# Performance work log

Measured on AMD Instinct MI355X. Metric: run time of the kernel, lower is better.

The kernel has to match this reference:

```python
import jax, jax.numpy as jnp
import numpy as np

B, S, D = 4, 1024, 2048
H, KVH, HD = 32, 8, 64
N_REP = H // KVH  # 4
ROPE_THETA = 1000000.0


def _rope_tables(seq_len, head_dim, theta):
    inv_freq = 1.0 / (theta ** (np.arange(0, head_dim, 2, dtype=np.float32) / head_dim))
    t = np.arange(seq_len, dtype=np.float32)
    freqs = np.outer(t, inv_freq)                      # (S, HD/2)
    emb = np.concatenate([freqs, freqs], axis=-1)      # (S, HD)
    return jnp.asarray(np.cos(emb)), jnp.asarray(np.sin(emb))


def setup_inputs() -> dict:
    key = jax.random.key(0)
    kx, kq, kk, kv, ko = jax.random.split(key, 5)
    cos, sin = _rope_tables(S, HD, ROPE_THETA)
    s = 0.02
    return {
        "x": jax.random.normal(kx, (B, S, D), jnp.float32),
        "cos": cos,
        "sin": sin,
        "Wq": jax.random.normal(kq, (D, H * HD), jnp.float32) * s,
        "Wk": jax.random.normal(kk, (D, KVH * HD), jnp.float32) * s,
        "Wv": jax.random.normal(kv, (D, KVH * HD), jnp.float32) * s,
        "Wo": jax.random.normal(ko, (H * HD, D), jnp.float32) * s,
    }


def _rotate_half(t):
    t1, t2 = jnp.split(t, 2, axis=-1)
    return jnp.concatenate([-t2, t1], axis=-1)


def reference(x, cos, sin, Wq, Wk, Wv, Wo):
    # projections
    q = (x @ Wq).reshape(B, S, H, HD)      # (b, s, h, d)
    k = (x @ Wk).reshape(B, S, KVH, HD)
    v = (x @ Wv).reshape(B, S, KVH, HD)

    # RoPE: cos/sin (s, d) broadcast over heads (unsqueeze_dim=1 -> (s,1,d))
    c = cos[:, None, :]
    sn = sin[:, None, :]
    q = q * c + _rotate_half(q) * sn
    k = k * c + _rotate_half(k) * sn

    # GQA attention without physically repeating KV:
    # q grouped as (b, kvh, n_rep, s, d); repeat_kv '(h r)' maps q head g*n_rep+r -> kv head g
    qg = q.transpose(0, 2, 1, 3).reshape(B, KVH, N_REP, S, HD)
    kt = k.transpose(0, 2, 1, 3)  # (b, kvh, s, d)
    vt = v.transpose(0, 2, 1, 3)

    scale = 1.0 / jnp.sqrt(jnp.asarray(HD, x.dtype))
    scores = jnp.einsum('bgrqd,bgkd->bgrqk', qg, kt) * scale  # (b, kvh, rep, s, s)
    probs = jax.nn.softmax(scores, axis=-1)
    out = jnp.einsum('bgrqk,bgkd->bgrqd', probs, vt)           # (b, kvh, rep, s, d)

    out = out.reshape(B, H, S, HD).transpose(0, 2, 1, 3).reshape(B, S, H * HD)
    return out @ Wo
```

## Files before the change

### kernel.cpp

```cpp
#include <hip/hip_runtime.h>

typedef unsigned short u16;
typedef __attribute__((ext_vector_type(8))) __bf16 bf16x8;
typedef __attribute__((ext_vector_type(4))) _Float16 f16x4;
typedef __attribute__((ext_vector_type(8))) _Float16 f16x8;
typedef __attribute__((ext_vector_type(4))) float f32x4;

#define BB 4
#define SS 1024
#define DD 2048
#define HH 32
#define KVHN 8
#define HDIM 64

__device__ __forceinline__ u16 f2b(float f) {
    union { float f; unsigned u; } v; v.f = f;
    unsigned r = v.u + 0x7FFFu + ((v.u >> 16) & 1u);
    return (u16)(r >> 16);
}
__device__ __forceinline__ float b2f(u16 h) {
    union { unsigned u; float f; } v; v.u = ((unsigned)h) << 16; return v.f;
}

__device__ __forceinline__ f32x4 mfma16(bf16x8 a, bf16x8 b, f32x4 c) {
    return __builtin_amdgcn_mfma_f32_16x16x32_bf16(a, b, c, 0, 0, 0);
}
__device__ __forceinline__ f32x4 mfma16h(f16x8 a, f16x8 b, f32x4 c) {
    return __builtin_amdgcn_mfma_f32_16x16x32_f16(a, b, c, 0, 0, 0);
}

__device__ __forceinline__ void async_cp16(const void* g, void* l) {
    __builtin_amdgcn_global_load_lds((__attribute__((address_space(1))) void*)g,
                                     (__attribute__((address_space(3))) void*)l,
                                     16, 0, 0);
}

__device__ __forceinline__ void block_sync() {
    asm volatile("" ::: "memory");
    __builtin_amdgcn_s_barrier();
    asm volatile("" ::: "memory");
}

__device__ __forceinline__ f16x8 pack8_f16(const float* p) {
    union { unsigned u[4]; f16x8 v; } pu;
    pu.u[0] = __builtin_bit_cast(unsigned, __builtin_amdgcn_cvt_pkrtz(p[0], p[1]));
    pu.u[1] = __builtin_bit_cast(unsigned, __builtin_amdgcn_cvt_pkrtz(p[2], p[3]));
    pu.u[2] = __builtin_bit_cast(unsigned, __builtin_amdgcn_cvt_pkrtz(p[4], p[5]));
    pu.u[3] = __builtin_bit_cast(unsigned, __builtin_amdgcn_cvt_pkrtz(p[6], p[7]));
    return pu.v;
}

__global__ __launch_bounds__(256) void prep_kernel(const float* __restrict__ x,
                                                   const float* __restrict__ Wq,
                                                   const float* __restrict__ Wk,
                                                   const float* __restrict__ Wv,
                                                   const float* __restrict__ Wo,
                                                   u16* __restrict__ xb,
                                                   u16* __restrict__ Wqkvt,
                                                   u16* __restrict__ Wot) {
    __shared__ float tile[32][33];
    int z = blockIdx.z;
    int tid = threadIdx.x;
    if (z == 4) {
        int lb = blockIdx.y * 64 + blockIdx.x;
        int i = (lb * 256 + tid) * 8;
        float4 v0 = *(const float4*)(x + i);
        float4 v1 = *(const float4*)(x + i + 4);
        uint4 r;
        r.x = (unsigned)f2b(v0.x) | ((unsigned)f2b(v0.y) << 16);
        r.y = (unsigned)f2b(v0.z) | ((unsigned)f2b(v0.w) << 16);
        r.z = (unsigned)f2b(v1.x) | ((unsigned)f2b(v1.y) << 16);
        r.w = (unsigned)f2b(v1.z) | ((unsigned)f2b(v1.w) << 16);
        *(uint4*)(xb + i) = r;
        return;
    }
    const float* W = (z == 0) ? Wq : (z == 1) ? Wk : (z == 2) ? Wv : Wo;
    int N = (z == 1 || z == 2) ? 512 : 2048;
    int n_off = (z == 1) ? 2048 : (z == 2) ? 2560 : 0;
    u16* Wt = (z == 3) ? Wot : Wqkvt;
    int n0 = blockIdx.x * 32;
    if (n0 >= N) return;
    int k0 = blockIdx.y * 32;
    int nj = tid & 31;
    int ki = tid >> 5;
#pragma unroll
    for (int it = 0; it < 4; it++) {
        int kk = it * 8 + ki;
        tile[kk][nj] = W[(size_t)(k0 + kk) * N + n0 + nj];
    }
    __syncthreads();
    int kp = tid & 15;
    int nn8 = tid >> 4;
#pragma unroll
    for (int pass = 0; pass < 2; pass++) {
        int nn = pass * 16 + nn8;
        unsigned v = (unsigned)f2b(tile[kp * 2][nn]) |
                     ((unsigned)f2b(tile[kp * 2 + 1][nn]) << 16);
        *(unsigned*)&Wt[(size_t)(n0 + nn + n_off) * 2048 + k0 + kp * 2] = v;
    }
}

__global__ __launch_bounds__(512, 2) void gemm_qkv(const u16* __restrict__ A,
                                                   const u16* __restrict__ Bt,
                                                   const float* __restrict__ cosT,
                                                   const float* __restrict__ sinT,
                                                   u16* __restrict__ Qh,
                                                   u16* __restrict__ Kh,
                                                   u16* __restrict__ Vbuf) {
    __shared__ __align__(16) u16 Ls[2][32768];
    const int tid = threadIdx.x;
    const int lane = tid & 63;
    const int w = tid >> 6;

    const int bid = blockIdx.x;
    const int xcd = bid & 7;
    const int loc = bid >> 3;
    const int mt = (xcd & 3) * 4 + (loc & 3);
    const int nt = (xcd >> 2) * 6 + (loc >> 2);
    const int m0 = mt * 256;
    const int n0 = nt * 256;

    const int wm_h = w >> 2;
    const int wn = (w & 3) * 64;
    const int lr = lane & 15;
    const int lg = lane >> 4;

    const int sr = lane >> 3;
    const int sl = (lane & 7) ^ (sr & 7);
    const u16* pA = A + (size_t)(m0 + w * 8 + sr) * 2048 + sl * 8;
    const u16* pB = Bt + (size_t)(n0 + w * 8 + sr) * 2048 + sl * 8;

#define STA(buf_, h_, kt_)                                                               \
    {                                                                                    \
        async_cp16(pA + (size_t)((h_) * 128) * 2048 + (kt_) * 64, &Ls[buf_][(h_) * 8192 + w * 512]);            \
        async_cp16(pA + (size_t)((h_) * 128 + 64) * 2048 + (kt_) * 64, &Ls[buf_][(h_) * 8192 + 4096 + w * 512]); \
    }
#define STB(buf_, h_, kt_)                                                               \
    {                                                                                    \
        async_cp16(pB + (size_t)((h_) * 128) * 2048 + (kt_) * 64, &Ls[buf_][16384 + (h_) * 8192 + w * 512]);            \
        async_cp16(pB + (size_t)((h_) * 128 + 64) * 2048 + (kt_) * 64, &Ls[buf_][16384 + (h_) * 8192 + 4096 + w * 512]); \
    }

    f32x4 acc[8][4];
    const f32x4 zero4 = {0.f, 0.f, 0.f, 0.f};
#pragma unroll
    for (int i = 0; i < 8; i++)
#pragma unroll
        for (int j = 0; j < 4; j++) acc[i][j] = zero4;

    bf16x8 af[8], b0[4], b1[4];

#define LDA(mh_, buf_)                                                                   \
    _Pragma("unroll") for (int mi = 0; mi < 4; mi++) _Pragma("unroll") for (int ks = 0; ks < 2; ks++) { \
        int rh = (mh_) * 64 + mi * 16 + lr;                                              \
        af[mi * 2 + ks] = *(const bf16x8*)(&Ls[buf_][wm_h * 8192 + rh * 64 + (((ks * 4 + lg) ^ (lr & 7)) * 8)]); \
    }
#define LDB(dst_, nh_, buf_)                                                             \
    _Pragma("unroll") for (int ni = 0; ni < 2; ni++) _Pragma("unroll") for (int ks = 0; ks < 2; ks++) { \
        int rowb = wn + (nh_) * 32 + ni * 16 + lr;                                       \
        dst_[ni * 2 + ks] = *(const bf16x8*)(&Ls[buf_][16384 + (rowb >> 7) * 8192 + (rowb & 127) * 64 + (((ks * 4 + lg) ^ (lr & 7)) * 8)]); \
    }
#define QMM(mh_, nh_, bb_)                                                               \
    __builtin_amdgcn_s_setprio(1);                                                       \
    _Pragma("unroll") for (int mi = 0; mi < 4; mi++) _Pragma("unroll") for (int ni = 0; ni < 2; ni++) { \
        acc[(mh_) * 4 + mi][(nh_) * 2 + ni] = mfma16(af[mi * 2 + 0], bb_[ni * 2 + 0], acc[(mh_) * 4 + mi][(nh_) * 2 + ni]); \
        acc[(mh_) * 4 + mi][(nh_) * 2 + ni] = mfma16(af[mi * 2 + 1], bb_[ni * 2 + 1], acc[(mh_) * 4 + mi][(nh_) * 2 + ni]); \
    }                                                                                    \
    __builtin_amdgcn_s_setprio(0);
#define WAITLDS                                                                          \
    asm volatile("s_waitcnt lgkmcnt(0)" ::: "memory");                                   \
    __builtin_amdgcn_sched_barrier(0);

    STA(0, 0, 0); STA(0, 1, 0); STB(0, 0, 0); STB(0, 1, 0);
    STB(1, 0, 1); STB(1, 1, 1);
    asm volatile("s_waitcnt vmcnt(0)" ::: "memory");
    block_sync();

#pragma unroll 1
    for (int I = 0; I < 16; ++I) {
        const int tb = 2 * I + 1;
        const int ta2 = (2 * I + 2) & 31;
        const int tb2 = (2 * I + 3) & 31;

        LDA(0, 0); LDB(b0, 0, 0);
        STA(1, 0, tb);
        block_sync(); WAITLDS;
        QMM(0, 0, b0);
        block_sync();

        LDB(b1, 1, 0);
        STA(1, 1, tb);
        block_sync(); WAITLDS;
        QMM(0, 1, b1);
        block_sync();

        LDA(1, 0);
        STB(0, 0, ta2);
        block_sync(); WAITLDS;
        QMM(1, 1, b1);
        block_sync();

        STB(0, 1, ta2);
        block_sync(); WAITLDS;
        QMM(1, 0, b0);
        asm volatile("s_waitcnt vmcnt(4)" ::: "memory");
        block_sync();

        LDA(0, 1); LDB(b0, 0, 1);
        STA(0, 0, ta2);
        block_sync(); WAITLDS;
        QMM(0, 0, b0);
        block_sync();

        LDB(b1, 1, 1);
        STA(0, 1, ta2);
        block_sync(); WAITLDS;
        QMM(0, 1, b1);
        block_sync();

        LDA(1, 1);
        STB(1, 0, tb2);
        block_sync(); WAITLDS;
        QMM(1, 1, b1);
        block_sync();

        STB(1, 1, tb2);
        block_sync(); WAITLDS;
        QMM(1, 0, b0);
        asm volatile("s_waitcnt vmcnt(4)" ::: "memory");
        block_sync();
    }
    asm volatile("s_waitcnt vmcnt(0)" ::: "memory");

    const int lq = lg * 4;
    const int wm = wm_h * 128;
    const int hb = (n0 + wn) >> 6;

    if (hb < 32) {
        const float QSC = 0.125f * 1.44269504088896f;
#pragma unroll
        for (int mi = 0; mi < 8; mi++)
#pragma unroll
            for (int i = 0; i < 4; i++) {
                int r = m0 + wm + mi * 16 + lq + i;
                int s = r & (SS - 1);
                int b = r >> 10;
                const float* cb = cosT + s * HDIM;
                const float* sb = sinT + s * HDIM;
                u16* drow = Qh + ((size_t)(b * HH + hb) * SS + s) * HDIM;
#pragma unroll
                for (int p = 0; p < 2; p++) {
                    int dlo = p * 16 + lr;
                    float c = cb[dlo], sn = sb[dlo];
                    float alo = acc[mi][p][i], ahi = acc[mi][p + 2][i];
                    drow[dlo]      = f2b((alo * c - ahi * sn) * QSC);
                    drow[dlo + 32] = f2b((ahi * c + alo * sn) * QSC);
                }
            }
    } else if (hb < 40) {
        int g = hb - 32;
#pragma unroll
        for (int mi = 0; mi < 8; mi++)
#pragma unroll
            for (int i = 0; i < 4; i++) {
                int r = m0 + wm + mi * 16 + lq + i;
                int s = r & (SS - 1);
                int b = r >> 10;
                int rr = s & 7;
                int kpos = (s & ~31) + ((rr >= 4) ? 16 : 0) + ((s >> 3) & 3) * 4 + (rr & 3);
                const float* cb = cosT + s * HDIM;
                const float* sb = sinT + s * HDIM;
                u16* drow = Kh + ((size_t)(b * KVHN + g) * SS + kpos) * HDIM;
#pragma unroll
                for (int p = 0; p < 2; p++) {
                    int dlo = p * 16 + lr;
                    float c = cb[dlo], sn = sb[dlo];
                    float alo = acc[mi][p][i], ahi = acc[mi][p + 2][i];
                    drow[dlo]      = f2b(alo * c - ahi * sn);
                    drow[dlo + 32] = f2b(ahi * c + alo * sn);
                }
            }
    } else {
        int cv0 = (n0 + wn) - 2560;
#pragma unroll
        for (int mi = 0; mi < 8; mi++)
#pragma unroll
            for (int ni = 0; ni < 4; ni++)
#pragma unroll
                for (int i = 0; i < 4; i++) {
                    int r = m0 + wm + mi * 16 + lq + i;
                    union { _Float16 h; u16 u; } cvu;
                    cvu.h = (_Float16)acc[mi][ni][i];
                    Vbuf[(size_t)r * 512 + cv0 + ni * 16 + lr] = cvu.u;
                }
    }
#undef STA
#undef STB
#undef LDA
#undef LDB
#undef QMM
#undef WAITLDS
}

__global__ __launch_bounds__(512, 2) void gemm_out(const u16* __restrict__ A,
                                                   const u16* __restrict__ Bt,
                                                   float* __restrict__ C) {
    __shared__ __align__(16) u16 Ls[2][24576];
    const int tid = threadIdx.x;
    const int lane = tid & 63;
    const int w = tid >> 6;

    const int bid = blockIdx.x;
    const int xcd = bid & 7;
    const int loc = bid >> 3;
    const int mt = (xcd & 3) * 4 + (loc & 3);
    const int nt = (xcd >> 2) * 8 + (loc >> 2);
    const int m0 = mt * 256;
    const int n0 = nt * 128;

    const int wm = (w >> 1) * 64;
    const int wn = (w & 1) * 64;
    const int lr = lane & 15;
    const int lg = lane >> 4;

    const int row0 = tid >> 2;
    const int g = tid & 3;
    const int sg = g ^ ((row0 >> 1) & 3);
    const u16* pA0 = A + (size_t)(m0 + row0) * 2048 + sg * 8;
    const u16* pA1 = pA0 + (size_t)128 * 2048;
    const u16* pB0 = Bt + (size_t)(n0 + row0) * 2048 + sg * 8;

#define OSTA(buf_, ks_, T_)                                                     \
    {                                                                           \
        async_cp16(pA0 + (T_) * 64 + (ks_) * 32, &Ls[buf_][(ks_) * 8192 + w * 512]);        \
        async_cp16(pA1 + (T_) * 64 + (ks_) * 32, &Ls[buf_][(ks_) * 8192 + 4096 + w * 512]); \
    }
#define OSTB(buf_, ks_, T_)                                                     \
    {                                                                           \
        async_cp16(pB0 + (T_) * 64 + (ks_) * 32, &Ls[buf_][16384 + (ks_) * 4096 + w * 512]); \
    }

    f32x4 acc[4][4];
    const f32x4 zero4 = {0.f, 0.f, 0.f, 0.f};
#pragma unroll
    for (int i = 0; i < 4; i++)
#pragma unroll
        for (int j = 0; j < 4; j++) acc[i][j] = zero4;

    bf16x8 af[4], bfr[4];

#define OLDA(ks_)                                                               \
    _Pragma("unroll") for (int mi = 0; mi < 4; mi++) {                          \
        int r_ = wm + mi * 16 + lr;                                             \
        af[mi] = *(const bf16x8*)(&Ls[cur][(ks_) * 8192 + r_ * 32 + ((lg ^ ((r_ >> 1) & 3)) * 8)]); \
    }
#define OLDB(ks_)                                                               \
    _Pragma("unroll") for (int ni = 0; ni < 4; ni++) {                          \
        int r_ = wn + ni * 16 + lr;                                             \
        bfr[ni] = *(const bf16x8*)(&Ls[cur][16384 + (ks_) * 4096 + r_ * 32 + ((lg ^ ((r_ >> 1) & 3)) * 8)]); \
    }
#define OMM                                                                     \
    __builtin_amdgcn_s_setprio(1);                                              \
    _Pragma("unroll") for (int mi = 0; mi < 4; mi++) _Pragma("unroll") for (int ni = 0; ni < 4; ni++) { \
        acc[mi][ni] = mfma16(af[mi], bfr[ni], acc[mi][ni]);                     \
    }                                                                           \
    __builtin_amdgcn_s_setprio(0);
#define OWAITMM                                                                 \
    asm volatile("s_waitcnt lgkmcnt(0)" ::: "memory");                          \
    __builtin_amdgcn_sched_barrier(0);

    OSTA(0, 0, 0); OSTB(0, 0, 0); OSTA(0, 1, 0); OSTB(0, 1, 0);
    OSTA(1, 0, 1); OSTB(1, 0, 1);
    asm volatile("s_waitcnt vmcnt(3)" ::: "memory");
    block_sync();

#pragma unroll 2
    for (int T = 0; T < 32; ++T) {
        const int cur = T & 1;
        const int oth = cur ^ 1;
        const int Tp1 = (T + 1) & 31;
        const int Tp2 = (T + 2) & 31;

        OLDA(0); OLDB(0);
        OSTA(oth, 1, Tp1); OSTB(oth, 1, Tp1);
        block_sync(); OWAITMM;
        OMM;
        block_sync();

        OLDA(1); OLDB(1);
        OSTA(cur, 0, Tp2); OSTB(cur, 0, Tp2);
        block_sync(); OWAITMM;
        OMM;
        asm volatile("s_waitcnt vmcnt(3)" ::: "memory");
        block_sync();
    }
    asm volatile("s_waitcnt vmcnt(0)" ::: "memory");

    const int lq = lg * 4;
#pragma unroll
    for (int mi = 0; mi < 4; mi++)
#pragma unroll
        for (int ni = 0; ni < 4; ni++)
#pragma unroll
            for (int i = 0; i < 4; i++) {
                int r = m0 + wm + mi * 16 + lq + i;
                int c = n0 + wn + ni * 16 + lr;
                C[(size_t)r * 2048 + c] = acc[mi][ni][i];
            }
#undef OSTA
#undef OSTB
#undef OLDA
#undef OLDB
#undef OMM
#undef OWAITMM
}

__global__ __launch_bounds__(256) void vtrans_kernel(const u16* __restrict__ Vbuf,
                                                     u16* __restrict__ Vt) {
    __shared__ u16 tile[64][65];
    int blk = blockIdx.x;
    int st = blk & 15;
    int t2 = blk >> 4;
    int g = t2 & 7;
    int b = t2 >> 3;
    int tid = threadIdx.x;
    int cj = tid & 63;
    int ri = tid >> 6;
    const u16* src = Vbuf + ((size_t)(b * SS + st * 64)) * 512 + g * 64;
#pragma unroll
    for (int it = 0; it < 16; it++) {
        int s_i = it * 4 + ri;
        tile[s_i][cj] = src[(size_t)s_i * 512 + cj];
    }
    __syncthreads();
    u16* dst = Vt + ((size_t)(b * KVHN + g) * HDIM) * SS + st * 64;
#pragma unroll
    for (int it = 0; it < 16; it++) {
        int hd_i = it * 4 + ri;
        dst[(size_t)hd_i * SS + cj] = tile[cj][hd_i];
    }
}

__global__ __launch_bounds__(256, 2) void flash_kernel(const u16* __restrict__ Qh,
                                                       const u16* __restrict__ Kh,
                                                       const u16* __restrict__ Vt,
                                                       u16* __restrict__ Attn) {
    __shared__ __align__(16) u16 Kls[2][4096];
    __shared__ __align__(16) u16 Vls[2][4096];
    const int tid = threadIdx.x;
    const int lane = tid & 63;
    const int w = tid >> 6;
    const int bid = blockIdx.x;
    const int gbp = ((bid & 7) << 2) | ((bid >> 3) & 3);
    const int qt2 = bid >> 5;
    const int g = gbp & 7;
    const int b = gbp >> 3;
    const int h = g * 4 + w;
    const int lr = lane & 15;
    const int lg = lane >> 4;
    const int lk8 = lg * 8;
    const int lq = lg * 4;

    const u16* Qbase = Qh + ((size_t)(b * HH + h) * SS + qt2 * 64) * HDIM;
    bf16x8 qb[4][2];
#pragma unroll
    for (int j = 0; j < 4; j++) {
        qb[j][0] = *(const bf16x8*)(Qbase + (size_t)(j * 16 + lr) * HDIM + lk8);
        qb[j][1] = *(const bf16x8*)(Qbase + (size_t)(j * 16 + lr) * HDIM + 32 + lk8);
    }

    const u16* Kbase = Kh + (size_t)(b * KVHN + g) * SS * HDIM;
    const u16* Vbase = Vt + (size_t)(b * KVHN + g) * HDIM * SS;

    const int r0 = tid >> 3;
    const int c0 = tid & 7;

    const f32x4 zero4 = {0.f, 0.f, 0.f, 0.f};
    const f32x4 initS = {-4.f, -4.f, -4.f, -4.f};
    f32x4 o[4][4];
    float lsum[4] = {0.f, 0.f, 0.f, 0.f};
#pragma unroll
    for (int j = 0; j < 4; j++)
#pragma unroll
        for (int i = 0; i < 4; i++) o[j][i] = zero4;

#define STAGE(kt, p)                                                              \
    {                                                                             \
        _Pragma("unroll") for (int sh = 0; sh < 2; sh++) {                        \
            int rr = r0 + sh * 32;                                                \
            int cs = c0 ^ (rr & 7);                                              \
            async_cp16(Kbase + (size_t)((kt) + rr) * HDIM + cs * 8,               \
                       &Kls[p][sh * 2048 + w * 512]);                             \
            async_cp16(Vbase + (size_t)rr * SS + (kt) + cs * 8,                   \
                       &Vls[p][sh * 2048 + w * 512]);                             \
        }                                                                         \
    }

    STAGE(0, 0);
    __syncthreads();

    for (int t = 0; t < 16; t++) {
        const int p = t & 1;
        if (t < 15) STAGE((t + 1) * 64, p ^ 1);

#pragma unroll
        for (int c = 0; c < 2; c++) {
            f32x4 s[2][4];
#pragma unroll
            for (int halfi = 0; halfi < 2; halfi++) {
                const int R = c * 32 + halfi * 16 + lr;
                const u16* kr = &Kls[p][R * 64];
                bf16x8 kb0 = *(const bf16x8*)(kr + ((lg ^ (R & 7)) * 8));
                bf16x8 kb1 = *(const bf16x8*)(kr + (((4 + lg) ^ (R & 7)) * 8));
#pragma unroll
                for (int j = 0; j < 4; j++) {
                    f32x4 a = initS;
                    a = mfma16(kb0, qb[j][0], a);
                    a = mfma16(kb1, qb[j][1], a);
                    s[halfi][j] = a;
                }
            }

            f16x8 va[4];
#pragma unroll
            for (int hdt = 0; hdt < 4; hdt++) {
                const int R2 = hdt * 16 + lr;
                va[hdt] = *(const f16x8*)(&Vls[p][R2 * 64 + (((c * 4 + lg) ^ (R2 & 7)) * 8)]);
            }

#pragma unroll
            for (int j = 0; j < 4; j++) {
                float pv[8];
#pragma unroll
                for (int r = 0; r < 4; r++) {
                    pv[r] = __builtin_amdgcn_exp2f(s[0][j][r]);
                    pv[4 + r] = __builtin_amdgcn_exp2f(s[1][j][r]);
                }
                lsum[j] += ((pv[0] + pv[1]) + (pv[2] + pv[3])) +
                           ((pv[4] + pv[5]) + (pv[6] + pv[7]));
                f16x8 pb = pack8_f16(pv);
#pragma unroll
                for (int hdt = 0; hdt < 4; hdt++)
                    o[j][hdt] = mfma16h(va[hdt], pb, o[j][hdt]);
            }
        }
        __syncthreads();
    }

#pragma unroll
    for (int j = 0; j < 4; j++) {
        float su = lsum[j];
        su += __shfl_xor(su, 16);
        su += __shfl_xor(su, 32);
        float inv = 1.f / su;
        u16* Ob = Attn + ((size_t)(b * SS + qt2 * 64 + j * 16 + lr)) * 2048 + h * 64;
#pragma unroll
        for (int hdt = 0; hdt < 4; hdt++) {
            unsigned r0p = (unsigned)f2b(o[j][hdt][0] * inv) | ((unsigned)f2b(o[j][hdt][1] * inv) << 16);
            unsigned r1p = (unsigned)f2b(o[j][hdt][2] * inv) | ((unsigned)f2b(o[j][hdt][3] * inv) << 16);
            *(uint2*)(Ob + hdt * 16 + lq) = make_uint2(r0p, r1p);
        }
    }
}

extern "C" void kernel_launch(void* const* d_in, const int* in_sizes, int n_in,
                              void* d_out, int out_size, void* d_ws, size_t ws_size,
                              hipStream_t stream) {
    (void)in_sizes; (void)n_in; (void)out_size; (void)ws_size;
    const float* x = (const float*)d_in[0];
    const float* cosT = (const float*)d_in[1];
    const float* sinT = (const float*)d_in[2];
    const float* Wq = (const float*)d_in[3];
    const float* Wk = (const float*)d_in[4];
    const float* Wv = (const float*)d_in[5];
    const float* Wo = (const float*)d_in[6];
    float* out = (float*)d_out;

    char* ws = (char*)d_ws;
    u16* Xb    = (u16*)(ws);
    u16* Wqkvt = (u16*)(ws + 16777216);
    u16* Wot   = (u16*)(ws + 29360128);
    u16* Vbuf  = (u16*)(ws + 37748736);
    u16* Qh    = (u16*)(ws + 62914560);
    u16* Kh    = (u16*)(ws + 79691776);
    u16* Vt    = (u16*)(ws + 83886080);
    u16* Attn  = (u16*)(ws + 88080384);

    prep_kernel<<<dim3(64, 64, 5), 256, 0, stream>>>(x, Wq, Wk, Wv, Wo, Xb, Wqkvt, Wot);

    gemm_qkv<<<192, 512, 0, stream>>>(Xb, Wqkvt, cosT, sinT, Qh, Kh, Vbuf);

    vtrans_kernel<<<512, 256, 0, stream>>>(Vbuf, Vt);

    flash_kernel<<<512, 256, 0, stream>>>(Qh, Kh, Vt, Attn);

    gemm_out<<<256, 512, 0, stream>>>(Attn, Wot, out);
}
```

Before: 258.6 us.

## Fuse V transpose into QKV GEMM epilogue via swizzled LDS staging

The V-tile epilogue of the QKV GEMM now stages fp16 results in shared memory with an XOR swizzle, then writes them transposed straight into the Vt layout with 16-byte vector stores. This removes the separate vtrans kernel launch and the round trip of the Vbuf intermediate through global memory. In exchange the epilogue gains an extra barrier and LDS reuse, and it relies on the main-loop LDS buffers being free at that point.

```diff
diff --git a/kernel.cpp b/kernel.cpp
--- a/kernel.cpp
+++ b/kernel.cpp
@@ -20,6 +20,9 @@
 }
 __device__ __forceinline__ float b2f(u16 h) {
     union { unsigned u; float f; } v; v.u = ((unsigned)h) << 16; return v.f;
+}
+__device__ __forceinline__ u16 f2h(float f) {
+    union { _Float16 h; u16 u; } v; v.h = (_Float16)f; return v.u;
 }
 
 __device__ __forceinline__ f32x4 mfma16(bf16x8 a, bf16x8 b, f32x4 c) {
@@ -106,7 +109,7 @@
                                                    const float* __restrict__ sinT,
                                                    u16* __restrict__ Qh,
                                                    u16* __restrict__ Kh,
-                                                   u16* __restrict__ Vbuf) {
+                                                   u16* __restrict__ Vt) {
     __shared__ __align__(16) u16 Ls[2][32768];
     const int tid = threadIdx.x;
     const int lane = tid & 63;
@@ -281,18 +284,39 @@
                 }
             }
     } else {
-        int cv0 = (n0 + wn) - 2560;
-#pragma unroll
-        for (int mi = 0; mi < 8; mi++)
-#pragma unroll
-            for (int ni = 0; ni < 4; ni++)
-#pragma unroll
-                for (int i = 0; i < 4; i++) {
-                    int r = m0 + wm + mi * 16 + lq + i;
-                    union { _Float16 h; u16 u; } cvu;
-                    cvu.h = (_Float16)acc[mi][ni][i];
-                    Vbuf[(size_t)r * 512 + cv0 + ni * 16 + lr] = cvu.u;
-                }
+        char* LsT = (char*)&Ls[0][0];
+        const int dvb = n0 - 2560;
+#pragma unroll
+        for (int mi = 0; mi < 8; mi++) {
+            int gs = (wm >> 2) + mi * 4 + lg;
+#pragma unroll
+            for (int ni = 0; ni < 4; ni++) {
+                int dvl = wn + ni * 16 + lr;
+                int phys = gs ^ (dvl & 7);
+                union { u16 u[4]; uint2 v; } pk;
+                pk.u[0] = f2h(acc[mi][ni][0]);
+                pk.u[1] = f2h(acc[mi][ni][1]);
+                pk.u[2] = f2h(acc[mi][ni][2]);
+                pk.u[3] = f2h(acc[mi][ni][3]);
+                *(uint2*)(LsT + dvl * 512 + phys * 8) = pk.v;
+            }
+        }
+        block_sync();
+        const int bb = m0 >> 10;
+        const int sbase = m0 & 1023;
+#pragma unroll
+        for (int it = 0; it < 16; it++) {
+            int dvl = it * 16 + (tid >> 5);
+            int gs = (tid & 31) * 2;
+            int x = dvl & 7;
+            uint2 lo = *(const uint2*)(LsT + dvl * 512 + (gs ^ x) * 8);
+            uint2 hi = *(const uint2*)(LsT + dvl * 512 + ((gs + 1) ^ x) * 8);
+            int dvg = dvb + dvl;
+            int g = dvg >> 6;
+            int dd = dvg & 63;
+            u16* dst = Vt + ((size_t)(bb * KVHN + g) * HDIM + dd) * SS + sbase + (tid & 31) * 8;
+            *(uint4*)dst = make_uint4(lo.x, lo.y, hi.x, hi.y);
+        }
     }
 #undef STA
 #undef STB
@@ -413,32 +437,6 @@
 #undef OLDB
 #undef OMM
 #undef OWAITMM
-}
-
-__global__ __launch_bounds__(256) void vtrans_kernel(const u16* __restrict__ Vbuf,
-                                                     u16* __restrict__ Vt) {
-    __shared__ u16 tile[64][65];
-    int blk = blockIdx.x;
-    int st = blk & 15;
-    int t2 = blk >> 4;
-    int g = t2 & 7;
-    int b = t2 >> 3;
-    int tid = threadIdx.x;
-    int cj = tid & 63;
-    int ri = tid >> 6;
-    const u16* src = Vbuf + ((size_t)(b * SS + st * 64)) * 512 + g * 64;
-#pragma unroll
-    for (int it = 0; it < 16; it++) {
-        int s_i = it * 4 + ri;
-        tile[s_i][cj] = src[(size_t)s_i * 512 + cj];
-    }
-    __syncthreads();
-    u16* dst = Vt + ((size_t)(b * KVHN + g) * HDIM) * SS + st * 64;
-#pragma unroll
-    for (int it = 0; it < 16; it++) {
-        int hd_i = it * 4 + ri;
-        dst[(size_t)hd_i * SS + cj] = tile[cj][hd_i];
-    }
 }
 
 __global__ __launch_bounds__(256, 2) void flash_kernel(const u16* __restrict__ Qh,
@@ -580,7 +578,6 @@
     u16* Xb    = (u16*)(ws);
     u16* Wqkvt = (u16*)(ws + 16777216);
     u16* Wot   = (u16*)(ws + 29360128);
-    u16* Vbuf  = (u16*)(ws + 37748736);
     u16* Qh    = (u16*)(ws + 62914560);
     u16* Kh    = (u16*)(ws + 79691776);
     u16* Vt    = (u16*)(ws + 83886080);
@@ -588,9 +585,7 @@
 
     prep_kernel<<<dim3(64, 64, 5), 256, 0, stream>>>(x, Wq, Wk, Wv, Wo, Xb, Wqkvt, Wot);
 
-    gemm_qkv<<<192, 512, 0, stream>>>(Xb, Wqkvt, cosT, sinT, Qh, Kh, Vbuf);
-
-    vtrans_kernel<<<512, 256, 0, stream>>>(Vbuf, Vt);
+    gemm_qkv<<<192, 512, 0, stream>>>(Xb, Wqkvt, cosT, sinT, Qh, Kh, Vt);
 
     flash_kernel<<<512, 256, 0, stream>>>(Qh, Kh, Vt, Attn);
 
```

New measurement: 255.0 us. About the same (-1.4%).
